# Kernel optimization log

Hardware: AMD Instinct MI355X
Metric: run time of the kernel (lower is better)

Reference implementation:

```python
import jax, jax.numpy as jnp
import numpy as np

STRIDE, PADDING, EPS = 2, 1, 1e-5


def setup_inputs() -> dict:
    key = jax.random.key(0)
    k1, k2, k3 = jax.random.split(key, 3)
    C_in, C_out, K = 64, 64, 4
    x = jax.random.normal(k1, (32, C_in, 64, 64), dtype=jnp.float32)
    weight = jax.random.normal(k2, (C_in, C_out, K, K), dtype=jnp.float32) * 0.05  # torch layout (in,out,kh,kw)
    conv_bias = jax.random.normal(k3, (C_out,), dtype=jnp.float32) * 0.02
    gamma = jnp.ones((C_out,), dtype=jnp.float32)
    beta = jnp.zeros((C_out,), dtype=jnp.float32)
    running_mean = jnp.zeros((C_out,), dtype=jnp.float32)
    running_var = jnp.ones((C_out,), dtype=jnp.float32)
    return {"x": x, "weight": weight, "conv_bias": conv_bias, "gamma": gamma,
            "beta": beta, "running_mean": running_mean, "running_var": running_var}


def _conv_transpose2d(x, weight, bias, stride, padding):
    # torch.nn.functional.conv_transpose2d equivalent:
    # conv with lhs_dilation=stride, spatially-flipped kernel, in/out axes swapped,
    # and padding k-1-p on each side.
    k = weight.shape[2]
    w_t = jnp.transpose(jnp.flip(weight, (2, 3)), (1, 0, 2, 3))  # (Cout, Cin, k, k)
    pad = k - 1 - padding
    y = jax.lax.conv_general_dilated(
        x, w_t,
        window_strides=(1, 1),
        padding=[(pad, pad), (pad, pad)],
        lhs_dilation=(stride, stride),
        dimension_numbers=("NCHW", "OIHW", "NCHW"),
    )
    return y + bias[None, :, None, None]


def reference(x, weight, conv_bias, gamma, beta, running_mean, running_var):
    # ConvTranspose2d
    y = _conv_transpose2d(x, weight, conv_bias, STRIDE, PADDING)  # [N,C,128,128]
    # BatchNorm2d (inference, running stats)
    scale = gamma * jax.lax.rsqrt(running_var + EPS)
    y = (y - running_mean[None, :, None, None]) * scale[None, :, None, None] + beta[None, :, None, None]
    # Softmax over channel dim
    y = jax.nn.softmax(y, axis=1)
    # MaxPool2d(k=2, s=2): H,W are even, so reshape-max is exact
    N, C, H, W = y.shape
    y = y.reshape(N, C, H // 2, 2, W // 2, 2).max(axis=(3, 5))  # [N,C,64,64]
    return y
```

## Files before the change

kernel.cpp:

```cpp
#include <hip/hip_runtime.h>
#include <hip/hip_bf16.h>
#include <math.h>


typedef __attribute__((ext_vector_type(8))) short short8;
typedef __attribute__((ext_vector_type(4))) float floatx4;
typedef __attribute__((ext_vector_type(2))) unsigned uint2v;
typedef __attribute__((ext_vector_type(4))) unsigned uint4v;

__device__ ushort g_wfrag[4 * 8 * 4 * 64 * 8];
__device__ float g_aff[64];

#define L2E 1.44269504088896340736f

__device__ __forceinline__ ushort f2bf(float f) {
  union { float f; unsigned u; } v; v.f = f;
  unsigned r = v.u + 0x7FFF + ((v.u >> 16) & 1);
  return (ushort)(r >> 16);
}

__global__ __launch_bounds__(256) void prep_kernel(
    const float* __restrict__ w, const float* __restrict__ bias,
    const float* __restrict__ gamma, const float* __restrict__ beta,
    const float* __restrict__ mean, const float* __restrict__ var) {
  int t = blockIdx.x * 256 + threadIdx.x;
  int cin0 = (t >> 6) * 2;
  int cout = t & 63;
  int nt = cout >> 4, b15 = cout & 15;
  int q = (cin0 & 31) >> 3;
  int j = cin0 & 7;
  int ksq = cin0 >> 5;
  float Aw = gamma[cout] * rsqrtf(var[cout] + 1e-5f) * L2E;

  const float4* p0 = (const float4*)&w[(cin0 * 64 + cout) * 16];
  const float4* p1 = (const float4*)&w[((cin0 + 1) * 64 + cout) * 16];
  float a[16], b[16];
  {
    float4 f0 = p0[0], f1 = p0[1], f2 = p0[2], f3 = p0[3];
    a[0]=f0.x; a[1]=f0.y; a[2]=f0.z; a[3]=f0.w; a[4]=f1.x; a[5]=f1.y; a[6]=f1.z; a[7]=f1.w;
    a[8]=f2.x; a[9]=f2.y; a[10]=f2.z; a[11]=f2.w; a[12]=f3.x; a[13]=f3.y; a[14]=f3.z; a[15]=f3.w;
    float4 g0 = p1[0], g1 = p1[1], g2 = p1[2], g3 = p1[3];
    b[0]=g0.x; b[1]=g0.y; b[2]=g0.z; b[3]=g0.w; b[4]=g1.x; b[5]=g1.y; b[6]=g1.z; b[7]=g1.w;
    b[8]=g2.x; b[9]=g2.y; b[10]=g2.z; b[11]=g2.w; b[12]=g3.x; b[13]=g3.y; b[14]=g3.z; b[15]=g3.w;
  }
#pragma unroll
  for (int kh = 0; kh < 4; ++kh)
#pragma unroll
    for (int kw = 0; kw < 4; ++kw) {
      int r = (kh & 1) ? 0 : 1;
      int pp = (kw & 1) ? 0 : 1;
      int c = r * 2 + pp;
      int tap = (kh >> 1) * 2 + (kw >> 1);
      int ks = tap * 2 + ksq;
      unsigned u = (unsigned)f2bf(a[kh * 4 + kw] * Aw) |
                   ((unsigned)f2bf(b[kh * 4 + kw] * Aw) << 16);
      *(unsigned*)&g_wfrag[(((c * 8 + ks) * 4 + nt) * 64 + q * 16 + b15) * 8 + j] = u;
    }

  if (t < 64) {
    float A0 = gamma[t] * rsqrtf(var[t] + 1e-5f);
    g_aff[t] = ((bias[t] - mean[t]) * A0 + beta[t]) * L2E;
  }
}

__device__ __forceinline__ unsigned cvtpk(float a, float b) {
  unsigned r;
  asm("v_cvt_pk_bf16_f32 %0, %1, %2" : "=v"(r) : "v"(a), "v"(b));
  return r;
}

__device__ __forceinline__ short8 and8(short8 v, unsigned m) {
  union { short8 s; uint4v u; } x;
  x.s = v;
  x.u &= m;
  return x.s;
}

template <int CTRL>
__device__ __forceinline__ float dpp_add(float v) {
  unsigned t = (unsigned)__builtin_amdgcn_update_dpp(
      0, (int)__float_as_uint(v), CTRL, 0xF, 0xF, true);
  return v + __uint_as_float(t);
}

__device__ __forceinline__ float sum16(float v) {
  v = dpp_add<0xB1>(v);
  v = dpp_add<0x4E>(v);
  v = dpp_add<0x141>(v);
  v = dpp_add<0x140>(v);
  return v;
}

__device__ __forceinline__ float fexp2(float x) {
#if __has_builtin(__builtin_amdgcn_exp2f)
  return __builtin_amdgcn_exp2f(x);
#else
  return exp2f(x);
#endif
}

__global__ __launch_bounds__(512, 6) void fused_kernel(const float* __restrict__ x,
                                                       float* __restrict__ out) {
  __shared__ __align__(16) ushort xs[3 * 64 * 64];
  __shared__ __align__(16) float red[64 * 64];

  const int tid  = threadIdx.x;
  const int ph   = blockIdx.x;
  const int n    = blockIdx.y;
  const int wave = tid >> 6;
  const int lane = tid & 63;
  const int b15  = lane & 15;
  const int q    = lane >> 4;
  const int wc   = wave & 1;
  const int c    = wave >> 1;
  const int r    = c >> 1, p = c & 1;

  {
    float4 z = {0.f, 0.f, 0.f, 0.f};
    *(float4*)&red[tid * 8] = z;
    *(float4*)&red[tid * 8 + 4] = z;
  }

  for (int e = tid; e < 768; e += 512) {
    int iw4 = e & 15;
    int c4  = (e >> 4) & 15;
    int row = e >> 8;
    int ih  = ph - 1 + row;
    float4 v0 = {0.f, 0.f, 0.f, 0.f}, v1 = v0, v2 = v0, v3 = v0;
    if (ih >= 0 && ih < 64) {
      const float* xp = x + ((n * 64 + c4 * 4) * 64 + ih) * 64 + iw4 * 4;
      v0 = *(const float4*)xp;          v1 = *(const float4*)(xp + 4096);
      v2 = *(const float4*)(xp + 8192); v3 = *(const float4*)(xp + 12288);
    }
    int chunk = c4 >> 1, half4 = (c4 & 1) * 4;
    float cc[4][4] = {{v0.x, v1.x, v2.x, v3.x}, {v0.y, v1.y, v2.y, v3.y},
                      {v0.z, v1.z, v2.z, v3.z}, {v0.w, v1.w, v2.w, v3.w}};
#pragma unroll
    for (int ii = 0; ii < 4; ++ii) {
      int col = iw4 * 4 + ii;
      uint2v pk = {cvtpk(cc[ii][0], cc[ii][1]), cvtpk(cc[ii][2], cc[ii][3])};
      *(uint2v*)&xs[(row * 64 + col) * 64 + ((chunk ^ (col & 7)) * 8) + half4] = pk;
    }
  }

  float Dc[4];
#pragma unroll
  for (int nt = 0; nt < 4; ++nt) Dc[nt] = g_aff[nt * 16 + b15];

  const unsigned m_b0 = (p == 1 && wc == 1 && b15 == 15) ? 0u : ~0u;
  const unsigned m_b1 = (p == 0 && wc == 0 && b15 == 0) ? 0u : ~0u;

  int A_[2][2][2];
#pragma unroll
  for (int mt = 0; mt < 2; ++mt)
#pragma unroll
    for (int b = 0; b < 2; ++b) {
      int col = (wc * 32 + mt * 16 + b15 + (b ? p - 1 : p)) & 63;
#pragma unroll
      for (int par = 0; par < 2; ++par)
        A_[mt][b][par] = r * 4096 + col * 64 + (((par * 4 + q) ^ (col & 7)) * 8);
    }

  short8 bfA[4], bfB[4];
  {
    const short8* wf = (const short8*)g_wfrag + (c * 8) * 256;
#pragma unroll
    for (int nt = 0; nt < 4; ++nt) bfA[nt] = wf[nt * 64 + lane];
  }
  __syncthreads();

  floatx4 acc[8];
#pragma unroll
  for (int nt = 0; nt < 4; ++nt) {
    acc[nt]     = (floatx4){Dc[nt], Dc[nt], Dc[nt], Dc[nt]};
    acc[4 + nt] = (floatx4){Dc[nt], Dc[nt], Dc[nt], Dc[nt]};
  }

#pragma unroll
  for (int ks = 0; ks < 8; ++ks) {
    const int a = ks >> 2, b = (ks >> 1) & 1, par = ks & 1;
    short8* cur = (ks & 1) ? bfB : bfA;
    short8* nxt = (ks & 1) ? bfA : bfB;
    if (ks < 7) {
      const short8* wf = (const short8*)g_wfrag + (c * 8 + ks + 1) * 256;
#pragma unroll
      for (int nt = 0; nt < 4; ++nt) nxt[nt] = wf[nt * 64 + lane];
    }
    const int ho = a ? 0 : 4096;
    short8 af0 = *(const short8*)&xs[A_[0][b][par] + ho];
    short8 af1 = *(const short8*)&xs[A_[1][b][par] + ho];
    if (b == 0) af1 = and8(af1, m_b0);
    else        af0 = and8(af0, m_b1);
#pragma unroll
    for (int nt = 0; nt < 4; ++nt) {
      acc[nt]     = __builtin_amdgcn_mfma_f32_16x16x32_bf16(af0, cur[nt], acc[nt], 0, 0, 0);
      acc[4 + nt] = __builtin_amdgcn_mfma_f32_16x16x32_bf16(af1, cur[nt], acc[4 + nt], 0, 0, 0);
    }
  }

#pragma unroll
  for (int mt = 0; mt < 2; ++mt) {
    float sm[4] = {0.f, 0.f, 0.f, 0.f};
#pragma unroll
    for (int nt = 0; nt < 4; ++nt)
#pragma unroll
      for (int reg = 0; reg < 4; ++reg) {
        float e = fexp2(acc[mt * 4 + nt][reg]);
        acc[mt * 4 + nt][reg] = e;
        sm[reg] += e;
      }
#pragma unroll
    for (int reg = 0; reg < 4; ++reg)
      sm[reg] = __builtin_amdgcn_rcpf(sum16(sm[reg]));
    const int qb = wc * 8 + mt * 4 + q;
#pragma unroll
    for (int nt = 0; nt < 4; ++nt) {
      int cout = nt * 16 + b15;
      int idx = cout * 64 + ((qb ^ (cout & 7)) << 2);
#pragma unroll
      for (int reg = 0; reg < 4; ++reg)
        __hip_atomic_fetch_max(&red[idx + reg], acc[mt * 4 + nt][reg] * sm[reg],
                               __ATOMIC_RELAXED, __HIP_MEMORY_SCOPE_WORKGROUP);
    }
  }
  __syncthreads();

  for (int e = tid; e < 2048; e += 512) {
    int pw2  = e & 31;
    int cout = e >> 5;
    float2 val = *(float2*)&red[cout * 64 + (((pw2 >> 1) ^ (cout & 7)) << 2) + (pw2 & 1) * 2];
    *(float2*)&out[((n * 64 + cout) * 64 + ph) * 64 + pw2 * 2] = val;
  }
}

extern "C" void kernel_launch(void* const* d_in, const int* in_sizes, int n_in,
                              void* d_out, int out_size, void* d_ws, size_t ws_size,
                              hipStream_t stream) {
  const float* x     = (const float*)d_in[0];
  const float* w     = (const float*)d_in[1];
  const float* bias  = (const float*)d_in[2];
  const float* gamma = (const float*)d_in[3];
  const float* beta  = (const float*)d_in[4];
  const float* mean  = (const float*)d_in[5];
  const float* var   = (const float*)d_in[6];
  float* out = (float*)d_out;

  prep_kernel<<<8, 256, 0, stream>>>(w, bias, gamma, beta, mean, var);
  dim3 grid(64, 32);
  fused_kernel<<<grid, 512, 0, stream>>>(x, out);
}
```

Measured before the change: 129.0 us.

## Compute two pooled output rows per block to reuse input halo and weights

New measurement: 140.5 us. 1.09x slower.

```diff
diff --git a/kernel.cpp b/kernel.cpp
--- a/kernel.cpp
+++ b/kernel.cpp
@@ -99,13 +99,13 @@
 #endif
 }
 
-__global__ __launch_bounds__(512, 6) void fused_kernel(const float* __restrict__ x,
+__global__ __launch_bounds__(512, 4) void fused_kernel(const float* __restrict__ x,
                                                        float* __restrict__ out) {
-  __shared__ __align__(16) ushort xs[3 * 64 * 64];
-  __shared__ __align__(16) float red[64 * 64];
+  __shared__ __align__(16) ushort xs[4 * 64 * 64];
+  __shared__ __align__(16) float red[2 * 64 * 65];
 
   const int tid  = threadIdx.x;
-  const int ph   = blockIdx.x;
+  const int ph0  = blockIdx.x * 2;
   const int n    = blockIdx.y;
   const int wave = tid >> 6;
   const int lane = tid & 63;
@@ -117,15 +117,14 @@
 
   {
     float4 z = {0.f, 0.f, 0.f, 0.f};
-    *(float4*)&red[tid * 8] = z;
-    *(float4*)&red[tid * 8 + 4] = z;
-  }
-
-  for (int e = tid; e < 768; e += 512) {
+    for (int e = tid; e < 2080; e += 512) ((float4*)red)[e] = z;
+  }
+
+  for (int e = tid; e < 1024; e += 512) {
     int iw4 = e & 15;
     int c4  = (e >> 4) & 15;
     int row = e >> 8;
-    int ih  = ph - 1 + row;
+    int ih  = ph0 - 1 + row;
     float4 v0 = {0.f, 0.f, 0.f, 0.f}, v1 = v0, v2 = v0, v3 = v0;
     if (ih >= 0 && ih < 64) {
       const float* xp = x + ((n * 64 + c4 * 4) * 64 + ih) * 64 + iw4 * 4;
@@ -169,11 +168,11 @@
   }
   __syncthreads();
 
-  floatx4 acc[8];
-#pragma unroll
-  for (int nt = 0; nt < 4; ++nt) {
-    acc[nt]     = (floatx4){Dc[nt], Dc[nt], Dc[nt], Dc[nt]};
-    acc[4 + nt] = (floatx4){Dc[nt], Dc[nt], Dc[nt], Dc[nt]};
+  floatx4 acc[16];
+#pragma unroll
+  for (int i = 0; i < 16; ++i) {
+    float d = Dc[i & 3];
+    acc[i] = (floatx4){d, d, d, d};
   }
 
 #pragma unroll
@@ -186,50 +185,59 @@
 #pragma unroll
       for (int nt = 0; nt < 4; ++nt) nxt[nt] = wf[nt * 64 + lane];
     }
-    const int ho = a ? 0 : 4096;
-    short8 af0 = *(const short8*)&xs[A_[0][b][par] + ho];
-    short8 af1 = *(const short8*)&xs[A_[1][b][par] + ho];
-    if (b == 0) af1 = and8(af1, m_b0);
-    else        af0 = and8(af0, m_b1);
-#pragma unroll
-    for (int nt = 0; nt < 4; ++nt) {
-      acc[nt]     = __builtin_amdgcn_mfma_f32_16x16x32_bf16(af0, cur[nt], acc[nt], 0, 0, 0);
-      acc[4 + nt] = __builtin_amdgcn_mfma_f32_16x16x32_bf16(af1, cur[nt], acc[4 + nt], 0, 0, 0);
-    }
-  }
-
-#pragma unroll
-  for (int mt = 0; mt < 2; ++mt) {
-    float sm[4] = {0.f, 0.f, 0.f, 0.f};
-#pragma unroll
-    for (int nt = 0; nt < 4; ++nt)
-#pragma unroll
-      for (int reg = 0; reg < 4; ++reg) {
-        float e = fexp2(acc[mt * 4 + nt][reg]);
-        acc[mt * 4 + nt][reg] = e;
-        sm[reg] += e;
+    const int hb = a ? 0 : 4096;
+#pragma unroll
+    for (int prow = 0; prow < 2; ++prow) {
+      short8 a0 = *(const short8*)&xs[A_[0][b][par] + prow * 4096 + hb];
+      short8 a1 = *(const short8*)&xs[A_[1][b][par] + prow * 4096 + hb];
+      if (b == 0) a1 = and8(a1, m_b0);
+      else        a0 = and8(a0, m_b1);
+#pragma unroll
+      for (int nt = 0; nt < 4; ++nt) {
+        acc[prow * 8 + nt] =
+            __builtin_amdgcn_mfma_f32_16x16x32_bf16(a0, cur[nt], acc[prow * 8 + nt], 0, 0, 0);
+        acc[prow * 8 + 4 + nt] =
+            __builtin_amdgcn_mfma_f32_16x16x32_bf16(a1, cur[nt], acc[prow * 8 + 4 + nt], 0, 0, 0);
       }
-#pragma unroll
-    for (int reg = 0; reg < 4; ++reg)
-      sm[reg] = __builtin_amdgcn_rcpf(sum16(sm[reg]));
-    const int qb = wc * 8 + mt * 4 + q;
-#pragma unroll
-    for (int nt = 0; nt < 4; ++nt) {
-      int cout = nt * 16 + b15;
-      int idx = cout * 64 + ((qb ^ (cout & 7)) << 2);
+    }
+  }
+
+#pragma unroll
+  for (int prow = 0; prow < 2; ++prow)
+#pragma unroll
+    for (int mt = 0; mt < 2; ++mt) {
+      float sm[4] = {0.f, 0.f, 0.f, 0.f};
+#pragma unroll
+      for (int nt = 0; nt < 4; ++nt)
+#pragma unroll
+        for (int reg = 0; reg < 4; ++reg) {
+          float e = fexp2(acc[prow * 8 + mt * 4 + nt][reg]);
+          acc[prow * 8 + mt * 4 + nt][reg] = e;
+          sm[reg] += e;
+        }
 #pragma unroll
       for (int reg = 0; reg < 4; ++reg)
-        __hip_atomic_fetch_max(&red[idx + reg], acc[mt * 4 + nt][reg] * sm[reg],
-                               __ATOMIC_RELAXED, __HIP_MEMORY_SCOPE_WORKGROUP);
-    }
-  }
+        sm[reg] = __builtin_amdgcn_rcpf(sum16(sm[reg]));
+#pragma unroll
+      for (int nt = 0; nt < 4; ++nt) {
+        int idx = (prow * 64 + nt * 16 + b15) * 65 + wc * 32 + mt * 16 + q * 4;
+#pragma unroll
+        for (int reg = 0; reg < 4; ++reg) {
+          float v = acc[prow * 8 + mt * 4 + nt][reg] * sm[reg];
+          __hip_atomic_fetch_max((unsigned*)&red[idx + reg], __float_as_uint(v),
+                                 __ATOMIC_RELAXED, __HIP_MEMORY_SCOPE_WORKGROUP);
+        }
+      }
+    }
   __syncthreads();
 
   for (int e = tid; e < 2048; e += 512) {
-    int pw2  = e & 31;
-    int cout = e >> 5;
-    float2 val = *(float2*)&red[cout * 64 + (((pw2 >> 1) ^ (cout & 7)) << 2) + (pw2 & 1) * 2];
-    *(float2*)&out[((n * 64 + cout) * 64 + ph) * 64 + pw2 * 2] = val;
+    int pw4  = e & 15;
+    int cout = (e >> 4) & 63;
+    int rl   = e >> 10;
+    int base = (rl * 64 + cout) * 65 + pw4 * 4;
+    float4 v = {red[base], red[base + 1], red[base + 2], red[base + 3]};
+    *(float4*)&out[((n * 64 + cout) * 64 + (ph0 + rl)) * 64 + pw4 * 4] = v;
   }
 }
 
@@ -246,6 +254,6 @@
   float* out = (float*)d_out;
 
   prep_kernel<<<8, 256, 0, stream>>>(w, bias, gamma, beta, mean, var);
-  dim3 grid(64, 32);
+  dim3 grid(32, 32);
   fused_kernel<<<grid, 512, 0, stream>>>(x, out);
 }
```
